# Kernel tuning notes

Measured on AMD Instinct MI355X. Metric: run time of the kernel, lower is better.

## Reference

```python
import jax, jax.numpy as jnp
import numpy as np

POOL = (32, 32, 32)
P_ENC_DIM = 48
NON_LOCAL_ITER = 2


def _neighbor_graph(spatial):
    # connectivity=2 binary structure in 3x3x3 (k_size=3): 19 offsets with |dx|+|dy|+|dz| <= 2
    D, H, W = spatial
    offs = np.array([(dx, dy, dz) for dx in (-1, 0, 1) for dy in (-1, 0, 1) for dz in (-1, 0, 1)
                     if abs(dx) + abs(dy) + abs(dz) <= 2], dtype=np.int64)  # [K=19,3]
    coords = np.stack(np.meshgrid(np.arange(D), np.arange(H), np.arange(W), indexing='ij'), -1).reshape(-1, 3)
    nbr = coords[:, None, :] + offs[None]                                  # [N,K,3]
    valid = ((nbr >= 0) & (nbr < np.array([D, H, W]))).all(-1)             # [N,K] side nodes lose oob edges
    nbrc = np.clip(nbr, 0, np.array([D - 1, H - 1, W - 1]))
    idx = np.ravel_multi_index(nbrc.reshape(-1, 3).T, (D, H, W)).reshape(valid.shape)
    return jnp.asarray(idx, jnp.int32), jnp.asarray(valid)


def _build_pe(spatial, p_enc_dim, dtype=jnp.float32):
    # sin/cos positional encoding over 3D grid, interleaved per axis (build_geo_feature)
    D, H, W = spatial
    d_model = p_enc_dim // 3
    div = (1e-4) ** (jnp.arange(0, d_model, 2, dtype=dtype) / d_model)     # [d_model//2]
    grids = jnp.meshgrid(jnp.arange(D), jnp.arange(H), jnp.arange(W), indexing='ij')
    parts = []
    for d in range(3):
        ang = grids[d].astype(dtype)[None] * div[:, None, None, None]      # [h,D,H,W]
        parts.append(jnp.stack([jnp.sin(ang), jnp.cos(ang)], 1).reshape(d_model, D, H, W))
    pe = jnp.concatenate(parts, 0)                                         # [p_enc_dim,D,H,W]
    return pe.reshape(p_enc_dim, -1).T                                     # [N,p_enc_dim]


def setup_inputs():
    key = jax.random.key(0)
    ks = jax.random.split(key, 6)
    B, Cf, Cc, FD, GD = 2, 256, 21, 64, 64
    D, H, W = POOL
    neighbor_idx, nbr_mask = _neighbor_graph(POOL)

    def lin(k, fi, fo):
        return jax.random.normal(k, (fi, fo), jnp.float32) / np.sqrt(fi).astype(np.float32)

    return {
        'cam': jax.random.uniform(ks[0], (B, Cc, D, H, W), jnp.float32),
        'f': jax.random.normal(ks[1], (B, Cf, D, H, W), jnp.float32),
        'theta_w': lin(ks[2], Cf, FD), 'theta_b': jnp.zeros((FD,), jnp.float32),
        'phi_w': lin(ks[3], Cf, FD), 'phi_b': jnp.zeros((FD,), jnp.float32),
        'geo_theta_w': lin(ks[4], P_ENC_DIM, GD), 'geo_theta_b': jnp.zeros((GD,), jnp.float32),
        'geo_phi_w': lin(ks[5], P_ENC_DIM, GD), 'geo_phi_b': jnp.zeros((GD,), jnp.float32),
        'neighbor_idx': neighbor_idx, 'nbr_mask': nbr_mask,
    }


def reference(cam, f, theta_w, theta_b, phi_w, phi_b, geo_theta_w, geo_theta_b,
              geo_phi_w, geo_phi_b, neighbor_idx, nbr_mask):
    B, Cc, D, H, W = cam.shape
    N = D * H * W
    f_flat = f.reshape(B, f.shape[1], N).transpose(0, 2, 1)                # [B,N,Cf]
    x_theta = f_flat @ theta_w + theta_b                                    # [B,N,fd]
    x_phi = (f_flat @ phi_w + phi_b)[:, neighbor_idx]                       # [B,N,K,fd] gather
    pe = jax.lax.stop_gradient(_build_pe((D, H, W), P_ENC_DIM, cam.dtype))  # geo feature is detached
    g_theta = pe @ geo_theta_w + geo_theta_b                                # [N,gd]
    g_phi = (pe @ geo_phi_w + geo_phi_b)[neighbor_idx]                      # [N,K,gd]
    # merge_type 'scaled_dot_product_geo': f = theta.phi + geo_theta.geo_phi; softmax(f / sqrt(K))
    scores = jnp.einsum('bnd,bnkd->bnk', x_theta, x_phi) \
           + jnp.einsum('nd,nkd->nk', g_theta, g_phi)[None]
    Kn = scores.shape[-1]
    scores = scores / jnp.sqrt(jnp.asarray(Kn, scores.dtype))
    scores = jnp.where(nbr_mask[None], scores, -jnp.inf)                    # side nodes: fewer edges
    w = jax.nn.softmax(scores, axis=-1)                                     # [B,N,K]
    cam_flat = cam.reshape(B, Cc, N).transpose(0, 2, 1)                     # [B,N,Cc]
    for _ in range(NON_LOCAL_ITER):                                         # weights fixed (f unchanged)
        cam_flat = jnp.einsum('bnk,bnkc->bnc', w, cam_flat[:, neighbor_idx])
    return cam_flat.transpose(0, 2, 1).reshape(B, Cc, D, H, W)
```

## Files before the change

### kernel.cpp

```cpp
#include <hip/hip_runtime.h>
#include <hip/hip_bf16.h>
#include <hip/hip_fp16.h>

#define DD 32
#define HH 32
#define WW 32
#define NN 32768
#define BB 2
#define CF 256
#define CC 21
#define FD 64
#define KK 19

typedef __attribute__((ext_vector_type(8))) short bf16x8;
typedef __attribute__((ext_vector_type(4))) float f32x4;

__device__ const int OFF[19][3] = {
    {-1,-1, 0}, {-1, 0,-1}, {-1, 0, 0}, {-1, 0, 1}, {-1, 1, 0},
    { 0,-1,-1}, { 0,-1, 0}, { 0,-1, 1}, { 0, 0,-1}, { 0, 0, 0},
    { 0, 0, 1}, { 0, 1,-1}, { 0, 1, 0}, { 0, 1, 1},
    { 1,-1, 0}, { 1, 0,-1}, { 1, 0, 0}, { 1, 0, 1}, { 1, 1, 0}
};

__device__ __forceinline__ unsigned short f2bf(float x) {
    unsigned u = __float_as_uint(x);
    u += 0x7FFFu + ((u >> 16) & 1u);
    return (unsigned short)(u >> 16);
}
__device__ __forceinline__ float bf2f(unsigned short h) {
    return __uint_as_float((unsigned)h << 16);
}
#define QF(x) (((x) & 3) ^ (((x) >> 2) & 3))

__global__ __launch_bounds__(256) void tbl_kernel(
    const float* __restrict__ gtw, const float* __restrict__ gtb,
    const float* __restrict__ gpw, const float* __restrict__ gpb,
    const float* __restrict__ thw, const float* __restrict__ phw,
    float* __restrict__ Tg, uint4* __restrict__ whi, uint4* __restrict__ wlo)
{
    int blk = blockIdx.x, tid = threadIdx.x;
    if (blk >= 10) {
        int gid = (blk - 10) * 256 + tid;
        int col = gid & 127;
        int kb = (gid >> 7) & 3;
        int ks = gid >> 9;
        const float* src = (col < 64) ? (thw + col) : (phw + (col - 64));
        int kbase = ks * 32 + kb * 8;
        unsigned hi4[4], lo4[4];
#pragma unroll
        for (int e2 = 0; e2 < 4; ++e2) {
            float va = src[(kbase + 2 * e2) * 64];
            float vb = src[(kbase + 2 * e2 + 1) * 64];
            unsigned short ha = f2bf(va), hb = f2bf(vb);
            unsigned short la = f2bf(va - bf2f(ha)), lb = f2bf(vb - bf2f(hb));
            hi4[e2] = (unsigned)ha | ((unsigned)hb << 16);
            lo4[e2] = (unsigned)la | ((unsigned)lb << 16);
        }
        int idx = (ks * 4 + kb) * 128 + col;
        whi[idx] = make_uint4(hi4[0], hi4[1], hi4[2], hi4[3]);
        wlo[idx] = make_uint4(lo4[0], lo4[1], lo4[2], lo4[3]);
        return;
    }

    __shared__ float pe_s[32][16];
    for (int i = tid; i < 512; i += 256) {
        int c = i >> 4, q = i & 15;
        int ii = q >> 1;
        float div = expf(-9.210340371976184f * (float)ii * 0.125f);
        float ang = (float)c * div;
        pe_s[c][q] = (q & 1) ? cosf(ang) : sinf(ang);
    }
    __syncthreads();

    __shared__ float panels[6][32][65];
    int npan = (blk == 9) ? 6 : 2;
#pragma unroll 1
    for (int pp = 0; pp < npan; ++pp) {
        int axis, isP;
        if (blk == 9) { axis = pp % 3; isP = pp / 3; }
        else          { axis = (pp == 0) ? (blk / 3) : (blk % 3); isP = pp; }
        const float* W = isP ? gpw : gtw;
#pragma unroll
        for (int e = 0; e < 8; ++e) {
            int idx = e * 256 + tid;
            int c = idx >> 6, j = idx & 63;
            float acc = 0.f;
#pragma unroll
            for (int q = 0; q < 16; ++q)
                acc = fmaf(pe_s[c][q], W[(axis * 16 + q) * 64 + j], acc);
            panels[pp][c][j] = acc;
        }
    }
    __syncthreads();

    if (blk < 9) {
        bool tr = (blk == 6) || (blk == 7);
#pragma unroll
        for (int e = 0; e < 4; ++e) {
            int idx = e * 256 + tid;
            int x = idx >> 5, y = idx & 31;
            float s = 0.f;
#pragma unroll
            for (int j = 0; j < 64; ++j)
                s = fmaf(panels[0][x][j], panels[1][y][j], s);
            Tg[blk * 1024 + (tr ? (y * 32 + x) : (x * 32 + y))] = s;
        }
    } else {
        if (tid < 96) {
            int ax = tid >> 5, c = tid & 31;
            float s = 0.f;
#pragma unroll
            for (int j = 0; j < 64; ++j) s = fmaf(panels[ax][c][j], gpb[j], s);
            Tg[9216 + ax * 32 + c] = s;
        } else if (tid < 192) {
            int t2 = tid - 96;
            int ax = t2 >> 5, c = t2 & 31;
            float s = 0.f;
#pragma unroll
            for (int j = 0; j < 64; ++j) s = fmaf(gtb[j], panels[3 + ax][c][j], s);
            Tg[9312 + ax * 32 + c] = s;
        } else if (tid == 192) {
            float s = 0.f;
#pragma unroll
            for (int j = 0; j < 64; ++j) s = fmaf(gtb[j], gpb[j], s);
            Tg[9408] = s;
        }
    }
}

__global__ __launch_bounds__(256) void proj_kernel(
    const float* __restrict__ f,
    const uint4* __restrict__ whi, const uint4* __restrict__ wlo,
    const float* __restrict__ thb, const float* __restrict__ phb,
    float* __restrict__ theta, __half* __restrict__ phi)
{
    __shared__ __align__(16) unsigned short Ahi[128][4][8];
    __shared__ __align__(16) unsigned short Alo[128][4][8];
    __shared__ __align__(16) unsigned short Bhi[128][4][8];
    __shared__ __align__(16) unsigned short Blo[128][4][8];

    int tid = threadIdx.x;
    int b = blockIdx.x >> 8;
    int n0 = (blockIdx.x & 255) * 128;
    int wv = tid >> 6, lane = tid & 63;
    int wr = (wv >> 1) * 64, wc = (wv & 1) * 64;
    int fr = lane & 15, kb_r = lane >> 4;

    int srow = tid & 127;
    int kb0 = (tid >> 7) * 2;

    const float* fb = f + (size_t)b * CF * NN + n0;

    f32x4 acc[4][4];
#pragma unroll
    for (int mi = 0; mi < 4; ++mi)
#pragma unroll
        for (int ni = 0; ni < 4; ++ni) acc[mi][ni] = (f32x4){0.f, 0.f, 0.f, 0.f};

#pragma unroll 1
    for (int k0 = 0; k0 < CF; k0 += 32) {
#pragma unroll
        for (int i = 0; i < 2; ++i) {
            int kb = kb0 + i;
            const float* src = fb + (size_t)(k0 + kb * 8) * NN + srow;
            unsigned hi4[4], lo4[4];
#pragma unroll
            for (int e2 = 0; e2 < 4; ++e2) {
                float va = src[(size_t)(2 * e2) * NN];
                float vb = src[(size_t)(2 * e2 + 1) * NN];
                unsigned short ha = f2bf(va), hb = f2bf(vb);
                unsigned short la = f2bf(va - bf2f(ha)), lb = f2bf(vb - bf2f(hb));
                hi4[e2] = (unsigned)ha | ((unsigned)hb << 16);
                lo4[e2] = (unsigned)la | ((unsigned)lb << 16);
            }
            int slot = kb ^ QF(srow);
            *(uint4*)&Ahi[srow][slot][0] = make_uint4(hi4[0], hi4[1], hi4[2], hi4[3]);
            *(uint4*)&Alo[srow][slot][0] = make_uint4(lo4[0], lo4[1], lo4[2], lo4[3]);
        }
        {
            const uint4* wh = whi + (size_t)(k0 >> 5) * 4 * 128;
            const uint4* wl = wlo + (size_t)(k0 >> 5) * 4 * 128;
#pragma unroll
            for (int i = 0; i < 2; ++i) {
                int kb = kb0 + i;
                uint4 hh = wh[kb * 128 + srow];
                uint4 ll = wl[kb * 128 + srow];
                int slot = kb ^ QF(srow);
                *(uint4*)&Bhi[srow][slot][0] = hh;
                *(uint4*)&Blo[srow][slot][0] = ll;
            }
        }
        __syncthreads();
        bf16x8 ah[4], al[4], bh[4], bl[4];
#pragma unroll
        for (int mi = 0; mi < 4; ++mi) {
            int r = wr + mi * 16 + fr;
            int slot = kb_r ^ QF(r);
            ah[mi] = *(const bf16x8*)&Ahi[r][slot][0];
            al[mi] = *(const bf16x8*)&Alo[r][slot][0];
        }
#pragma unroll
        for (int ni = 0; ni < 4; ++ni) {
            int c = wc + ni * 16 + fr;
            int slot = kb_r ^ QF(c);
            bh[ni] = *(const bf16x8*)&Bhi[c][slot][0];
            bl[ni] = *(const bf16x8*)&Blo[c][slot][0];
        }
#pragma unroll
        for (int mi = 0; mi < 4; ++mi)
#pragma unroll
            for (int ni = 0; ni < 4; ++ni) {
                acc[mi][ni] = __builtin_amdgcn_mfma_f32_16x16x32_bf16(ah[mi], bh[ni], acc[mi][ni], 0, 0, 0);
                acc[mi][ni] = __builtin_amdgcn_mfma_f32_16x16x32_bf16(al[mi], bh[ni], acc[mi][ni], 0, 0, 0);
                acc[mi][ni] = __builtin_amdgcn_mfma_f32_16x16x32_bf16(ah[mi], bl[ni], acc[mi][ni], 0, 0, 0);
            }
        __syncthreads();
    }

#pragma unroll
    for (int ni = 0; ni < 4; ++ni) {
        int j = wc + ni * 16 + fr;
        if (j < 64) {
            float bj = thb[j];
            float* outp = theta + (size_t)b * NN * 64 + j;
#pragma unroll
            for (int mi = 0; mi < 4; ++mi) {
                int nbase = n0 + wr + mi * 16 + kb_r * 4;
#pragma unroll
                for (int r = 0; r < 4; ++r)
                    outp[(size_t)(nbase + r) * 64] = acc[mi][ni][r] + bj;
            }
        } else {
            float bj = phb[j - 64];
            __half* outp = phi + (size_t)b * NN * 64 + (j - 64);
#pragma unroll
            for (int mi = 0; mi < 4; ++mi) {
                int nbase = n0 + wr + mi * 16 + kb_r * 4;
#pragma unroll
                for (int r = 0; r < 4; ++r)
                    outp[(size_t)(nbase + r) * 64] = __float2half(acc[mi][ni][r] + bj);
            }
        }
    }
}

__global__ __launch_bounds__(256) void gsc_kernel(
    const float* __restrict__ Tg, float* __restrict__ gsc)
{
    __shared__ float Ts[9 * 1024];
    __shared__ float UVs[193];
    int tid = threadIdx.x;
#pragma unroll
    for (int i = 0; i < 9; ++i) {
        int idx = i * 1024 + tid;
        Ts[idx] = Tg[idx];
        Ts[idx + 256] = Tg[idx + 256];
        Ts[idx + 512] = Tg[idx + 512];
        Ts[idx + 768] = Tg[idx + 768];
    }
    if (tid < 193) UVs[tid] = Tg[9216 + tid];
    __syncthreads();

    int n = blockIdx.x * 256 + tid;
    int d = n >> 10, h = (n >> 5) & 31, w = n & 31;
    float Un = UVs[d] + UVs[32 + h] + UVs[64 + w] + UVs[192];
    const float rs = 0.2294157338705618f;

#pragma unroll
    for (int k = 0; k < KK; ++k) {
        int nd = d + OFF[k][0], nh = h + OFF[k][1], nw = w + OFF[k][2];
        bool valid = ((unsigned)nd < 32u) && ((unsigned)nh < 32u) && ((unsigned)nw < 32u);
        int ndc = min(max(nd, 0), 31), nhc = min(max(nh, 0), 31), nwc = min(max(nw, 0), 31);
        float g = Ts[0 * 1024 + d * 32 + ndc] + Ts[1 * 1024 + d * 32 + nhc]
                + Ts[2 * 1024 + d * 32 + nwc] + Ts[3 * 1024 + h * 32 + ndc]
                + Ts[4 * 1024 + h * 32 + nhc] + Ts[5 * 1024 + h * 32 + nwc]
                + Ts[6 * 1024 + ndc * 32 + w] + Ts[7 * 1024 + nhc * 32 + w]
                + Ts[8 * 1024 + w * 32 + nwc]
                + Un + UVs[96 + ndc] + UVs[128 + nhc] + UVs[160 + nwc];
        gsc[(size_t)k * NN + n] = valid ? g * rs : -INFINITY;
    }
}

__global__ __launch_bounds__(256) void score_kernel(
    const float* __restrict__ theta, const __half* __restrict__ phi,
    const float* __restrict__ gsc, float* __restrict__ wgt)
{
    int tid = threadIdx.x;
    int lane = tid & 63;
    int wv = tid >> 6;
    int sub = lane >> 4;
    int col4 = lane & 15;
    int gn = blockIdx.x * 16 + wv * 4 + sub;
    int b = gn >> 15;
    int n = gn & (NN - 1);
    int d = n >> 10, h = (n >> 5) & 31, w = n & 31;

    float4 tq = *(const float4*)(theta + (size_t)gn * 64 + col4 * 4);
    const __half* pb = phi + (size_t)b * NN * 64;
    const float* gr = gsc + n;
    const float rs = 0.2294157338705618f;

    float s[KK];
#pragma unroll
    for (int k = 0; k < KK; ++k) {
        int nd = d + OFF[k][0], nh = h + OFF[k][1], nw = w + OFF[k][2];
        nd = min(max(nd, 0), 31); nh = min(max(nh, 0), 31); nw = min(max(nw, 0), 31);
        int nn = (nd << 10) + (nh << 5) + nw;
        uint2 raw = *(const uint2*)(pb + (size_t)nn * 64 + col4 * 4);
        __half2 h01 = __builtin_bit_cast(__half2, raw.x);
        __half2 h23 = __builtin_bit_cast(__half2, raw.y);
        float2 f01 = __half22float2(h01), f23 = __half22float2(h23);
        float part = tq.x * f01.x + tq.y * f01.y + tq.z * f23.x + tq.w * f23.y;
        part += __shfl_xor(part, 1, 16);
        part += __shfl_xor(part, 2, 16);
        part += __shfl_xor(part, 4, 16);
        part += __shfl_xor(part, 8, 16);
        s[k] = fmaf(part, rs, gr[(size_t)k * NN]);
    }
    float m = s[0];
#pragma unroll
    for (int k = 1; k < KK; ++k) m = fmaxf(m, s[k]);
    float sum = 0.f;
#pragma unroll
    for (int k = 0; k < KK; ++k) { s[k] = __expf(s[k] - m); sum += s[k]; }
    float inv = 1.f / sum;
#pragma unroll
    for (int kk2 = 0; kk2 < 2; ++kk2) {
        int k = kk2 * 16 + col4;
        if (k < KK) wgt[((size_t)b * KK + k) * NN + n] = s[k] * inv;
    }
}

__global__ __launch_bounds__(256) void prop_kernel(
    const float* __restrict__ cin, const float* __restrict__ wgt,
    float* __restrict__ cout)
{
    int gid = blockIdx.x * 256 + threadIdx.x;
    int n = gid & (NN - 1);
    int bc = gid >> 15;
    int b = bc / CC, c = bc % CC;
    int d = n >> 10, h = (n >> 5) & 31, w = n & 31;
    float acc = 0.f;
    const float* wb = wgt + (size_t)b * KK * NN;
    const float* cb = cin + ((size_t)b * CC + c) * NN;
#pragma unroll
    for (int k = 0; k < KK; ++k) {
        int nd = d + OFF[k][0], nh = h + OFF[k][1], nw = w + OFF[k][2];
        nd = min(max(nd, 0), 31); nh = min(max(nh, 0), 31); nw = min(max(nw, 0), 31);
        int nn = (nd << 10) + (nh << 5) + nw;
        acc += wb[(size_t)k * NN + n] * cb[nn];
    }
    cout[((size_t)b * CC + c) * NN + n] = acc;
}

extern "C" void kernel_launch(void* const* d_in, const int* in_sizes, int n_in,
                              void* d_out, int out_size, void* d_ws, size_t ws_size,
                              hipStream_t stream) {
    const float* cam = (const float*)d_in[0];
    const float* f   = (const float*)d_in[1];
    const float* thw = (const float*)d_in[2];
    const float* thb = (const float*)d_in[3];
    const float* phw = (const float*)d_in[4];
    const float* phb = (const float*)d_in[5];
    const float* gtw = (const float*)d_in[6];
    const float* gtb = (const float*)d_in[7];
    const float* gpw = (const float*)d_in[8];
    const float* gpb = (const float*)d_in[9];

    float*  ws    = (float*)d_ws;
    float*  theta = ws;
    __half* phi   = (__half*)(theta + (size_t)BB * NN * 64);
    float*  wgt   = (float*)((char*)phi + (size_t)BB * NN * 64 * 2);
    float*  gsc   = wgt + (size_t)BB * KK * NN;
    float*  cam1  = gsc + (size_t)KK * NN;
    uint4*  whi   = (uint4*)(cam1 + (size_t)BB * CC * NN);
    uint4*  wlo   = whi + 4096;
    float*  Tg    = (float*)(wlo + 4096);

    tbl_kernel<<<26, 256, 0, stream>>>(gtw, gtb, gpw, gpb, thw, phw, Tg, whi, wlo);
    proj_kernel<<<512, 256, 0, stream>>>(f, whi, wlo, thb, phb, theta, phi);
    gsc_kernel<<<NN / 256, 256, 0, stream>>>(Tg, gsc);
    score_kernel<<<BB * NN / 16, 256, 0, stream>>>(theta, phi, gsc, wgt);
    prop_kernel<<<BB * CC * NN / 256, 256, 0, stream>>>(cam, wgt, cam1);
    prop_kernel<<<BB * CC * NN / 256, 256, 0, stream>>>(cam1, wgt, (float*)d_out);
}
```

Before: 75.44 us.

## Double-buffer projection GEMM with direct global-to-LDS loads and smaller tiles

Rewrites the projection kernel so raw fp32 activations and the pre-split bf16 weights are copied straight into LDS with global_load_lds, double-buffered so the next K-slice loads while the current one runs MFMA. The hi/lo bf16 split of the activations moves from the global-load stage to after the LDS read. The tile shrinks from 128 to 64 rows, doubling the grid to 1024 blocks for more parallelism, and the weight table layout changes to match the new LDS addressing. The goal is to hide global memory latency and remove register staging, at the cost of repeating the conversion per wave and a more involved XOR swizzle whose bank-conflict behaviour is uncertain.

```diff
diff --git a/kernel.cpp b/kernel.cpp
--- a/kernel.cpp
+++ b/kernel.cpp
@@ -14,6 +14,7 @@
 
 typedef __attribute__((ext_vector_type(8))) short bf16x8;
 typedef __attribute__((ext_vector_type(4))) float f32x4;
+typedef __attribute__((ext_vector_type(4))) unsigned int u32x4;
 
 __device__ const int OFF[19][3] = {
     {-1,-1, 0}, {-1, 0,-1}, {-1, 0, 0}, {-1, 0, 1}, {-1, 1, 0},
@@ -30,7 +31,12 @@
 __device__ __forceinline__ float bf2f(unsigned short h) {
     return __uint_as_float((unsigned)h << 16);
 }
-#define QF(x) (((x) & 3) ^ (((x) >> 2) & 3))
+
+__device__ __forceinline__ void gl_lds16(const void* g, void* l) {
+    __builtin_amdgcn_global_load_lds(
+        (const __attribute__((address_space(1))) void*)g,
+        (__attribute__((address_space(3))) void*)l, 16, 0, 0);
+}
 
 __global__ __launch_bounds__(256) void tbl_kernel(
     const float* __restrict__ gtw, const float* __restrict__ gtb,
@@ -56,7 +62,7 @@
             hi4[e2] = (unsigned)ha | ((unsigned)hb << 16);
             lo4[e2] = (unsigned)la | ((unsigned)lb << 16);
         }
-        int idx = (ks * 4 + kb) * 128 + col;
+        int idx = ((ks * 128 + col) << 2) + kb;
         whi[idx] = make_uint4(hi4[0], hi4[1], hi4[2], hi4[3]);
         wlo[idx] = make_uint4(lo4[0], lo4[1], lo4[2], lo4[3]);
         return;
@@ -134,80 +140,86 @@
     const float* __restrict__ thb, const float* __restrict__ phb,
     float* __restrict__ theta, __half* __restrict__ phi)
 {
-    __shared__ __align__(16) unsigned short Ahi[128][4][8];
-    __shared__ __align__(16) unsigned short Alo[128][4][8];
-    __shared__ __align__(16) unsigned short Bhi[128][4][8];
-    __shared__ __align__(16) unsigned short Blo[128][4][8];
+    __shared__ __align__(16) float          Af[2][32 * 64];
+    __shared__ __align__(16) unsigned short Bh[2][512 * 8];
+    __shared__ __align__(16) unsigned short Bl[2][512 * 8];
 
     int tid = threadIdx.x;
-    int b = blockIdx.x >> 8;
-    int n0 = (blockIdx.x & 255) * 128;
+    int b = blockIdx.x >> 9;
+    int n0 = (blockIdx.x & 511) * 64;
     int wv = tid >> 6, lane = tid & 63;
-    int wr = (wv >> 1) * 64, wc = (wv & 1) * 64;
+    int wr = (wv & 1) * 32, wc = (wv >> 1) * 64;
     int fr = lane & 15, kb_r = lane >> 4;
 
-    int srow = tid & 127;
-    int kb0 = (tid >> 7) * 2;
-
     const float* fb = f + (size_t)b * CF * NN + n0;
 
-    f32x4 acc[4][4];
-#pragma unroll
-    for (int mi = 0; mi < 4; ++mi)
+    int a_kkoff = lane >> 4;
+    int a_p = lane & 15;
+    int b_coff = lane >> 2;
+    int b_kb = lane & 3;
+
+    f32x4 acc[2][4];
+#pragma unroll
+    for (int mi = 0; mi < 2; ++mi)
 #pragma unroll
         for (int ni = 0; ni < 4; ++ni) acc[mi][ni] = (f32x4){0.f, 0.f, 0.f, 0.f};
 
+#define STAGE(buf, ks)                                                         \
+    {                                                                          \
+        int k0s = (ks) * 32;                                                   \
+        _Pragma("unroll")                                                      \
+        for (int i = 0; i < 2; ++i) {                                          \
+            int kk0 = (wv * 2 + i) * 4;                                        \
+            int kk = kk0 + a_kkoff;                                            \
+            int kb = kk >> 3;                                                  \
+            const float* g = fb + (size_t)(k0s + kk) * NN + 4 * (a_p ^ (kb << 2)); \
+            gl_lds16(g, (void*)&Af[buf][kk0 * 64]);                            \
+        }                                                                      \
+        _Pragma("unroll")                                                      \
+        for (int i = 0; i < 2; ++i) {                                          \
+            int c0 = (wv * 2 + i) * 16;                                        \
+            size_t gidx = ((size_t)(ks) * 128 + c0 + b_coff) * 4 + b_kb;       \
+            gl_lds16(whi + gidx, (void*)&Bh[buf][c0 * 32]);                    \
+            gl_lds16(wlo + gidx, (void*)&Bl[buf][c0 * 32]);                    \
+        }                                                                      \
+    }
+
+    int cur = 0;
+    STAGE(0, 0);
+    __syncthreads();
+
 #pragma unroll 1
-    for (int k0 = 0; k0 < CF; k0 += 32) {
-#pragma unroll
-        for (int i = 0; i < 2; ++i) {
-            int kb = kb0 + i;
-            const float* src = fb + (size_t)(k0 + kb * 8) * NN + srow;
-            unsigned hi4[4], lo4[4];
+    for (int ks = 0; ks < 8; ++ks) {
+        if (ks < 7) STAGE(cur ^ 1, ks + 1);
+
+        bf16x8 ah[2], al[2], bh[4], bl[4];
+#pragma unroll
+        for (int mi = 0; mi < 2; ++mi) {
+            int prow = (wr + mi * 16 + fr) ^ (kb_r << 4);
+            float av[8];
+#pragma unroll
+            for (int j = 0; j < 8; ++j)
+                av[j] = Af[cur][(kb_r * 8 + j) * 64 + prow];
+            u32x4 h4, l4;
 #pragma unroll
             for (int e2 = 0; e2 < 4; ++e2) {
-                float va = src[(size_t)(2 * e2) * NN];
-                float vb = src[(size_t)(2 * e2 + 1) * NN];
+                float va = av[2 * e2], vb = av[2 * e2 + 1];
                 unsigned short ha = f2bf(va), hb = f2bf(vb);
                 unsigned short la = f2bf(va - bf2f(ha)), lb = f2bf(vb - bf2f(hb));
-                hi4[e2] = (unsigned)ha | ((unsigned)hb << 16);
-                lo4[e2] = (unsigned)la | ((unsigned)lb << 16);
+                h4[e2] = (unsigned)ha | ((unsigned)hb << 16);
+                l4[e2] = (unsigned)la | ((unsigned)lb << 16);
             }
-            int slot = kb ^ QF(srow);
-            *(uint4*)&Ahi[srow][slot][0] = make_uint4(hi4[0], hi4[1], hi4[2], hi4[3]);
-            *(uint4*)&Alo[srow][slot][0] = make_uint4(lo4[0], lo4[1], lo4[2], lo4[3]);
-        }
-        {
-            const uint4* wh = whi + (size_t)(k0 >> 5) * 4 * 128;
-            const uint4* wl = wlo + (size_t)(k0 >> 5) * 4 * 128;
-#pragma unroll
-            for (int i = 0; i < 2; ++i) {
-                int kb = kb0 + i;
-                uint4 hh = wh[kb * 128 + srow];
-                uint4 ll = wl[kb * 128 + srow];
-                int slot = kb ^ QF(srow);
-                *(uint4*)&Bhi[srow][slot][0] = hh;
-                *(uint4*)&Blo[srow][slot][0] = ll;
-            }
-        }
-        __syncthreads();
-        bf16x8 ah[4], al[4], bh[4], bl[4];
-#pragma unroll
-        for (int mi = 0; mi < 4; ++mi) {
-            int r = wr + mi * 16 + fr;
-            int slot = kb_r ^ QF(r);
-            ah[mi] = *(const bf16x8*)&Ahi[r][slot][0];
-            al[mi] = *(const bf16x8*)&Alo[r][slot][0];
+            ah[mi] = __builtin_bit_cast(bf16x8, h4);
+            al[mi] = __builtin_bit_cast(bf16x8, l4);
         }
 #pragma unroll
         for (int ni = 0; ni < 4; ++ni) {
-            int c = wc + ni * 16 + fr;
-            int slot = kb_r ^ QF(c);
-            bh[ni] = *(const bf16x8*)&Bhi[c][slot][0];
-            bl[ni] = *(const bf16x8*)&Blo[c][slot][0];
-        }
-#pragma unroll
-        for (int mi = 0; mi < 4; ++mi)
+            int e = ((wc + ni * 16 + fr) << 2) + kb_r;
+            bh[ni] = *(const bf16x8*)&Bh[cur][e * 8];
+            bl[ni] = *(const bf16x8*)&Bl[cur][e * 8];
+        }
+#pragma unroll
+        for (int mi = 0; mi < 2; ++mi)
 #pragma unroll
             for (int ni = 0; ni < 4; ++ni) {
                 acc[mi][ni] = __builtin_amdgcn_mfma_f32_16x16x32_bf16(ah[mi], bh[ni], acc[mi][ni], 0, 0, 0);
@@ -215,7 +227,9 @@
                 acc[mi][ni] = __builtin_amdgcn_mfma_f32_16x16x32_bf16(ah[mi], bl[ni], acc[mi][ni], 0, 0, 0);
             }
         __syncthreads();
-    }
+        cur ^= 1;
+    }
+#undef STAGE
 
 #pragma unroll
     for (int ni = 0; ni < 4; ++ni) {
@@ -224,7 +238,7 @@
             float bj = thb[j];
             float* outp = theta + (size_t)b * NN * 64 + j;
 #pragma unroll
-            for (int mi = 0; mi < 4; ++mi) {
+            for (int mi = 0; mi < 2; ++mi) {
                 int nbase = n0 + wr + mi * 16 + kb_r * 4;
 #pragma unroll
                 for (int r = 0; r < 4; ++r)
@@ -234,7 +248,7 @@
             float bj = phb[j - 64];
             __half* outp = phi + (size_t)b * NN * 64 + (j - 64);
 #pragma unroll
-            for (int mi = 0; mi < 4; ++mi) {
+            for (int mi = 0; mi < 2; ++mi) {
                 int nbase = n0 + wr + mi * 16 + kb_r * 4;
 #pragma unroll
                 for (int r = 0; r < 4; ++r)
@@ -378,7 +392,7 @@
     float*  Tg    = (float*)(wlo + 4096);
 
     tbl_kernel<<<26, 256, 0, stream>>>(gtw, gtb, gpw, gpb, thw, phw, Tg, whi, wlo);
-    proj_kernel<<<512, 256, 0, stream>>>(f, whi, wlo, thb, phb, theta, phi);
+    proj_kernel<<<1024, 256, 0, stream>>>(f, whi, wlo, thb, phb, theta, phi);
     gsc_kernel<<<NN / 256, 256, 0, stream>>>(Tg, gsc);
     score_kernel<<<BB * NN / 16, 256, 0, stream>>>(theta, phi, gsc, wgt);
     prop_kernel<<<BB * CC * NN / 256, 256, 0, stream>>>(cam, wgt, cam1);
```

Result: slower. 78.97 us (+4.7%).
